# Kernel tuning notes

Hardware: AMD Instinct MI355X
Metric: run time of the kernel (lower is better)

## Reference

```python
import jax, jax.numpy as jnp
import numpy as np

N, E, F_IN, F_OUT, K, T = 100_000, 1_600_000, 64, 64, 2, 2


def setup_inputs() -> dict:
    key = jax.random.key(0)
    ks = jax.random.split(key, 7)
    s = 0.1
    return {
        "x": jax.random.normal(ks[0], (N, F_IN), jnp.float32),
        "edge_index": jax.random.randint(ks[1], (2, E), 0, N, dtype=jnp.int32),
        "edge_weight": jax.random.uniform(ks[2], (E,), jnp.float32),
        "init_weight": (jax.random.normal(ks[3], (K, F_IN, F_OUT), jnp.float32) * s),
        "weight": (jax.random.normal(ks[4], (T - 1, K, F_OUT, F_OUT), jnp.float32) * s),
        "root_weight": (jax.random.normal(ks[5], (T, K, F_IN, F_OUT), jnp.float32) * s),
        "bias": (jax.random.normal(ks[6], (T, K, F_OUT), jnp.float32) * s),
    }


def _gcn_norm(row, col, edge_weight, n):
    # PyG ARMAConv: gcn_norm with add_self_loops=False; degree on dst (col).
    deg = jax.ops.segment_sum(edge_weight, col, num_segments=n)
    dinv = jnp.where(deg > 0, jax.lax.rsqrt(jnp.maximum(deg, 1e-12)), 0.0)
    return dinv[row] * edge_weight * dinv[col]


def _propagate(out, row, col, norm, n):
    # out: [K, N, F] -> gather src rows, scale by norm, scatter-add at dst.
    msgs = out[:, row, :] * norm[None, :, None]  # [K, E, F]
    return jax.vmap(lambda m: jax.ops.segment_sum(m, col, num_segments=n))(msgs)


def reference(x, edge_index, edge_weight, init_weight, weight, root_weight, bias):
    n = x.shape[0]
    row, col = edge_index[0], edge_index[1]
    norm = _gcn_norm(row, col, edge_weight, n)
    out = x
    for t in range(T):
        if t == 0:
            out = jnp.einsum('nf,kfo->kno', x, init_weight)  # [K,N,F_out]
        else:
            out = jnp.einsum('kno,kop->knp', out, weight[t - 1])
        out = _propagate(out, row, col, norm, n)
        root = jnp.einsum('nf,kfo->kno', x, root_weight[t])  # dropout p=0 / eval
        out = jax.nn.relu(out + root + bias[t][:, None, :])
    return out.mean(axis=0)  # mean over stacks -> [N, F_out]
```

## Files before the change

### kernel.cpp

```cpp
#include <hip/hip_runtime.h>

#define NN 100000
#define EE 1600000
#define FF 64
#define KK 2

#define NBKT 391
#define BKW 256
#define CAP 8192
#define EPB 6250
#define P2CAP 6144

#define FIX 68719476736.0f
#define FIXINV (1.0/68719476736.0)

typedef unsigned long long ull;
typedef __attribute__((ext_vector_type(8))) short bf16x8;
typedef __attribute__((ext_vector_type(4))) float f32x4;
typedef __attribute__((ext_vector_type(2))) float f32x2;

__device__ inline unsigned pack_bf16x2(float a, float b) {
    unsigned ua = __float_as_uint(a), ub = __float_as_uint(b);
    ua = (ua + 0x7FFFu + ((ua >> 16) & 1u)) >> 16;
    ub = (ub + 0x7FFFu + ((ub >> 16) & 1u)) >> 16;
    return ua | (ub << 16);
}
__device__ inline float bf_lo(unsigned u) { return __uint_as_float(u << 16); }
__device__ inline float bf_hi(unsigned u) { return __uint_as_float(u & 0xFFFF0000u); }
__device__ inline short bf16_of(float f) {
    unsigned u = __float_as_uint(f);
    u = (u + 0x7FFFu + ((u >> 16) & 1u)) >> 16;
    return (short)u;
}
__device__ inline unsigned bf16_bits(float f) {
    unsigned u = __float_as_uint(f);
    return (u + 0x7FFFu + ((u >> 16) & 1u)) >> 16;
}
__device__ inline unsigned short fp8x2_of(float a, float b) {
    int p = __builtin_amdgcn_cvt_pk_fp8_f32(a, b, 0, false);
    return (unsigned short)(p & 0xFFFF);
}

__device__ inline bf16x8 load_bfrag(const float* __restrict__ W, int col, int kg, int c) {
    bf16x8 f;
    #pragma unroll
    for (int i = 0; i < 8; ++i)
        f[i] = bf16_of(W[(c*32 + kg*8 + i)*FF + col]);
    return f;
}

__global__ __launch_bounds__(512) void k_p1(const int* __restrict__ row,
                                            const int* __restrict__ col,
                                            const float* __restrict__ ew,
                                            int* __restrict__ gcnt,
                                            uint2* __restrict__ records) {
    __shared__ uint2 srt[EPB];
    __shared__ int colsS[EPB];
    __shared__ int histo[NBKT];
    __shared__ int lbase[NBKT];
    __shared__ int gbase[NBKT];
    __shared__ int cur[NBKT];
    __shared__ int tmp[512];
    int tid = threadIdx.x;
    for (int i = tid; i < NBKT; i += 512) histo[i] = 0;
    __syncthreads();
    int s0 = blockIdx.x * EPB;
    #pragma unroll 1
    for (int r = 0; r < 13; ++r) {
        int t = r*512 + tid;
        if (t < EPB) {
            int c = col[s0 + t];
            colsS[t] = c;
            atomicAdd(&histo[c >> 8], 1);
        }
    }
    __syncthreads();
    int v = (tid < NBKT) ? histo[tid] : 0;
    tmp[tid] = v;
    __syncthreads();
    #pragma unroll
    for (int s = 1; s < 512; s <<= 1) {
        int t = (tid >= s) ? tmp[tid - s] : 0;
        __syncthreads();
        tmp[tid] += t;
        __syncthreads();
    }
    if (tid < NBKT) {
        int ex = tmp[tid] - v;
        lbase[tid] = ex;
        cur[tid] = ex;
        gbase[tid] = atomicAdd(&gcnt[tid], v);
    }
    __syncthreads();
    #pragma unroll 1
    for (int r = 0; r < 13; ++r) {
        int t = r*512 + tid;
        if (t < EPB) {
            int i = s0 + t;
            int c = colsS[t];
            int b = c >> 8;
            int slot = atomicAdd(&cur[b], 1);
            srt[slot] = make_uint2(((unsigned)row[i] << 8) | (unsigned)(c & 255),
                                   __float_as_uint(ew[i]));
        }
    }
    __syncthreads();
    int wid = tid >> 6, lane = tid & 63;
    for (int b = wid; b < NBKT; b += 8) {
        int n = histo[b], lb = lbase[b];
        size_t gb = (size_t)b*CAP + gbase[b];
        for (int i = lane; i < n; i += 64) records[gb + i] = srt[lb + i];
    }
}

__global__ __launch_bounds__(512) void k_p2(const int* __restrict__ gcnt,
                                            const uint2* __restrict__ records,
                                            int* __restrict__ off,
                                            float* __restrict__ dinv,
                                            unsigned* __restrict__ edat) {
    __shared__ uint2 rstage[P2CAP];
    __shared__ ull hd[BKW];
    __shared__ int loff[BKW];
    __shared__ int cur[BKW];
    __shared__ int tmp[512];
    int tid = threadIdx.x;
    int b = blockIdx.x;
    int cnt = gcnt[b];
    int v = (tid < NBKT) ? gcnt[tid] : 0;
    tmp[tid] = v;
    __syncthreads();
    #pragma unroll
    for (int s = 1; s < 512; s <<= 1) {
        int t = (tid >= s) ? tmp[tid - s] : 0;
        __syncthreads();
        tmp[tid] += t;
        __syncthreads();
    }
    int obase = tmp[b] - cnt;
    if (b == 0 && tid == 0) off[NN] = EE;
    if (tid < BKW) hd[tid] = 0ull;
    __syncthreads();
    size_t rbase = (size_t)b * CAP;
    for (int j = tid; j < cnt; j += 512) {
        uint2 rec = records[rbase + j];
        if (j < P2CAP) rstage[j] = rec;
        int c8 = rec.x & 255;
        atomicAdd(&hd[c8], (1ull << 48) | (ull)(__uint_as_float(rec.y) * FIX));
    }
    __syncthreads();
    int hv = (tid < BKW) ? (int)(hd[tid] >> 48) : 0;
    tmp[tid] = hv;
    __syncthreads();
    #pragma unroll
    for (int s = 1; s < 512; s <<= 1) {
        int t = (tid >= s) ? tmp[tid - s] : 0;
        __syncthreads();
        tmp[tid] += t;
        __syncthreads();
    }
    if (tid < BKW) {
        int excl = tmp[tid] - hv;
        loff[tid] = excl;
        cur[tid] = excl;
        int node = b*BKW + tid;
        if (node < NN) {
            off[node] = obase + excl;
            float d = (float)((double)(hd[tid] & 0xFFFFFFFFFFFFull) * FIXINV);
            dinv[node] = d > 0.f ? rsqrtf(fmaxf(d, 1e-12f)) : 0.f;
        }
    }
    __syncthreads();
    for (int j = tid; j < cnt; j += 512) {
        uint2 rec = (j < P2CAP) ? rstage[j] : records[rbase + j];
        int c8 = rec.x & 255;
        int slot = atomicAdd(&cur[c8], 1);
        edat[obase + slot] = ((rec.x >> 8) << 15) |
                             (bf16_bits(__uint_as_float(rec.y)) & 0x7FFFu);
    }
}

__global__ __launch_bounds__(256) void k_proj3(const float* __restrict__ x,
                                               const float* __restrict__ iw,
                                               const float* __restrict__ rw,
                                               const float* __restrict__ bias,
                                               const float* __restrict__ dsc,
                                               unsigned short* __restrict__ hbf8,
                                               unsigned* __restrict__ rbf0,
                                               unsigned* __restrict__ rbf1) {
    int lane = threadIdx.x & 63, wid = threadIdx.x >> 6;
    int col16 = lane & 15, kg = lane >> 4;
    int col = wid*16 + col16;

    bf16x8 Bi[2][2], B0[2][2], B1[2][2];
    #pragma unroll
    for (int k = 0; k < 2; ++k)
        #pragma unroll
        for (int c = 0; c < 2; ++c) {
            Bi[k][c] = load_bfrag(iw + k*4096, col, kg, c);
            B0[k][c] = load_bfrag(rw + k*4096, col, kg, c);
            B1[k][c] = load_bfrag(rw + (2 + k)*4096, col, kg, c);
        }
    float b00 = bias[col],        b01 = bias[FF + col];
    float b10 = bias[2*FF + col], b11 = bias[3*FF + col];

    int base = blockIdx.x * 64;
    #pragma unroll
    for (int s = 0; s < 4; ++s) {
        int arow = base + s*16 + col16;
        if (arow >= NN) arow = NN - 1;
        const float* xp = x + arow*FF + kg*8;
        float4 v0 = *(const float4*)xp;
        float4 v1 = *(const float4*)(xp + 4);
        float4 v2 = *(const float4*)(xp + 32);
        float4 v3 = *(const float4*)(xp + 36);
        bf16x8 A0, A1;
        A0[0]=bf16_of(v0.x); A0[1]=bf16_of(v0.y); A0[2]=bf16_of(v0.z); A0[3]=bf16_of(v0.w);
        A0[4]=bf16_of(v1.x); A0[5]=bf16_of(v1.y); A0[6]=bf16_of(v1.z); A0[7]=bf16_of(v1.w);
        A1[0]=bf16_of(v2.x); A1[1]=bf16_of(v2.y); A1[2]=bf16_of(v2.z); A1[3]=bf16_of(v2.w);
        A1[4]=bf16_of(v3.x); A1[5]=bf16_of(v3.y); A1[6]=bf16_of(v3.z); A1[7]=bf16_of(v3.w);

        f32x4 hi0 = {0.f,0.f,0.f,0.f}, hi1 = {0.f,0.f,0.f,0.f};
        hi0 = __builtin_amdgcn_mfma_f32_16x16x32_bf16(A0, Bi[0][0], hi0, 0, 0, 0);
        hi0 = __builtin_amdgcn_mfma_f32_16x16x32_bf16(A1, Bi[0][1], hi0, 0, 0, 0);
        hi1 = __builtin_amdgcn_mfma_f32_16x16x32_bf16(A0, Bi[1][0], hi1, 0, 0, 0);
        hi1 = __builtin_amdgcn_mfma_f32_16x16x32_bf16(A1, Bi[1][1], hi1, 0, 0, 0);
        f32x4 r00 = {b00,b00,b00,b00}, r01 = {b01,b01,b01,b01};
        r00 = __builtin_amdgcn_mfma_f32_16x16x32_bf16(A0, B0[0][0], r00, 0, 0, 0);
        r00 = __builtin_amdgcn_mfma_f32_16x16x32_bf16(A1, B0[0][1], r00, 0, 0, 0);
        r01 = __builtin_amdgcn_mfma_f32_16x16x32_bf16(A0, B0[1][0], r01, 0, 0, 0);
        r01 = __builtin_amdgcn_mfma_f32_16x16x32_bf16(A1, B0[1][1], r01, 0, 0, 0);
        f32x4 r10 = {b10,b10,b10,b10}, r11 = {b11,b11,b11,b11};
        r10 = __builtin_amdgcn_mfma_f32_16x16x32_bf16(A0, B1[0][0], r10, 0, 0, 0);
        r10 = __builtin_amdgcn_mfma_f32_16x16x32_bf16(A1, B1[0][1], r10, 0, 0, 0);
        r11 = __builtin_amdgcn_mfma_f32_16x16x32_bf16(A0, B1[1][0], r11, 0, 0, 0);
        r11 = __builtin_amdgcn_mfma_f32_16x16x32_bf16(A1, B1[1][1], r11, 0, 0, 0);
        #pragma unroll
        for (int r = 0; r < 4; ++r) {
            int node = base + s*16 + kg*4 + r;
            if (node < NN) {
                float f = dsc[node];
                hbf8[(node<<6) + col]  = fp8x2_of(hi0[r]*f, hi1[r]*f);
                rbf0[(node<<6) + col] = pack_bf16x2(r00[r], r01[r]);
                rbf1[(node<<6) + col] = pack_bf16x2(r10[r], r11[r]);
            }
        }
    }
}

__global__ __launch_bounds__(256) void k_mml(const unsigned* __restrict__ in,
                                             const float* __restrict__ W,
                                             const float* __restrict__ dsc,
                                             unsigned short* __restrict__ outp8) {
    int lane = threadIdx.x & 63, wid = threadIdx.x >> 6;
    int col16 = lane & 15, kg = lane >> 4;
    int col = wid*16 + col16;

    bf16x8 B0[2], B1[2];
    #pragma unroll
    for (int c = 0; c < 2; ++c) {
        B0[c] = load_bfrag(W, col, kg, c);
        B1[c] = load_bfrag(W + 4096, col, kg, c);
    }
    int base = blockIdx.x * 64;
    #pragma unroll
    for (int s = 0; s < 4; ++s) {
        int arow = base + s*16 + col16;
        if (arow >= NN) arow = NN - 1;
        const unsigned* ip = in + arow*FF + kg*8;
        uint4 u0 = *(const uint4*)ip;
        uint4 u1 = *(const uint4*)(ip + 4);
        uint4 u2 = *(const uint4*)(ip + 32);
        uint4 u3 = *(const uint4*)(ip + 36);
        unsigned uu[16] = {u0.x,u0.y,u0.z,u0.w, u1.x,u1.y,u1.z,u1.w,
                           u2.x,u2.y,u2.z,u2.w, u3.x,u3.y,u3.z,u3.w};
        bf16x8 A00, A01, A10, A11;
        #pragma unroll
        for (int i = 0; i < 8; ++i) {
            A00[i] = (short)(uu[i] & 0xFFFFu);      A10[i] = (short)(uu[i] >> 16);
            A01[i] = (short)(uu[8+i] & 0xFFFFu);    A11[i] = (short)(uu[8+i] >> 16);
        }
        f32x4 a0 = {0.f, 0.f, 0.f, 0.f};
        f32x4 a1 = {0.f, 0.f, 0.f, 0.f};
        a0 = __builtin_amdgcn_mfma_f32_16x16x32_bf16(A00, B0[0], a0, 0, 0, 0);
        a0 = __builtin_amdgcn_mfma_f32_16x16x32_bf16(A01, B0[1], a0, 0, 0, 0);
        a1 = __builtin_amdgcn_mfma_f32_16x16x32_bf16(A10, B1[0], a1, 0, 0, 0);
        a1 = __builtin_amdgcn_mfma_f32_16x16x32_bf16(A11, B1[1], a1, 0, 0, 0);
        #pragma unroll
        for (int r = 0; r < 4; ++r) {
            int node = base + s*16 + kg*4 + r;
            if (node < NN) {
                float f = dsc[node];
                outp8[(node<<6) + col] = fp8x2_of(a0[r]*f, a1[r]*f);
            }
        }
    }
}

__global__ __launch_bounds__(512) void k_pull(const int* __restrict__ off,
                                              const unsigned* __restrict__ edat,
                                              const unsigned short* __restrict__ hbf,
                                              const unsigned* __restrict__ rbf,
                                              const float* __restrict__ dinv,
                                              unsigned* __restrict__ out_bf,
                                              float* __restrict__ out_f32,
                                              int final_mean) {
    __shared__ unsigned ech[8][64];
    int lane = threadIdx.x & 63;
    int sub = threadIdx.x >> 6;
    int n0 = (blockIdx.x * 8 + sub) * 2;
    if (n0 >= NN) return;
    int n1 = n0 + 1;

    int beg = off[n0], mid = off[n0+1], end = off[n0+2];
    float dc0 = dinv[n0], dc1 = dinv[n1];
    unsigned rv0 = rbf[(n0<<6) + lane];
    unsigned rv1 = rbf[(n1<<6) + lane];

    float pa0=0.f,pa1=0.f,pb0=0.f,pb1=0.f,pc0=0.f,pc1=0.f,pd0=0.f,pd1=0.f;
    float qa0=0.f,qa1=0.f,qb0=0.f,qb1=0.f,qc0=0.f,qc1=0.f,qd0=0.f,qd1=0.f;

    for (int base = beg; base < end; base += 64) {
        int rem = end - base;
        int cc = rem < 64 ? rem : 64;
        ech[sub][lane] = (lane < cc) ? edat[base + lane] : 0u;
        __builtin_amdgcn_wave_barrier();
        int midrel = mid - base;
        if (midrel < 0) midrel = 0;
        if (midrel > 64) midrel = 64;
        int padded = (cc + 7) & ~7;
        for (int q = 0; q < padded; q += 8) {
            unsigned e[8];
            #pragma unroll
            for (int i = 0; i < 8; ++i) e[i] = ech[sub][q + i];
            unsigned us[8];
            #pragma unroll
            for (int i = 0; i < 8; ++i)
                us[i] = hbf[((e[i] >> 15) << 6) + lane];
            if (q + 8 <= midrel) {
                #pragma unroll
                for (int i = 0; i < 8; ++i) {
                    float w = __uint_as_float((e[i] & 0x7FFFu) << 16);
                    f32x2 h = __builtin_amdgcn_cvt_pk_f32_fp8(us[i], false);
                    if      ((i & 3) == 0) { pa0 = fmaf(w, h.x, pa0); pa1 = fmaf(w, h.y, pa1); }
                    else if ((i & 3) == 1) { pb0 = fmaf(w, h.x, pb0); pb1 = fmaf(w, h.y, pb1); }
                    else if ((i & 3) == 2) { pc0 = fmaf(w, h.x, pc0); pc1 = fmaf(w, h.y, pc1); }
                    else                   { pd0 = fmaf(w, h.x, pd0); pd1 = fmaf(w, h.y, pd1); }
                }
            } else if (q >= midrel) {
                #pragma unroll
                for (int i = 0; i < 8; ++i) {
                    float w = __uint_as_float((e[i] & 0x7FFFu) << 16);
                    f32x2 h = __builtin_amdgcn_cvt_pk_f32_fp8(us[i], false);
                    if      ((i & 3) == 0) { qa0 = fmaf(w, h.x, qa0); qa1 = fmaf(w, h.y, qa1); }
                    else if ((i & 3) == 1) { qb0 = fmaf(w, h.x, qb0); qb1 = fmaf(w, h.y, qb1); }
                    else if ((i & 3) == 2) { qc0 = fmaf(w, h.x, qc0); qc1 = fmaf(w, h.y, qc1); }
                    else                   { qd0 = fmaf(w, h.x, qd0); qd1 = fmaf(w, h.y, qd1); }
                }
            } else {
                #pragma unroll
                for (int i = 0; i < 8; ++i) {
                    float w = __uint_as_float((e[i] & 0x7FFFu) << 16);
                    f32x2 h = __builtin_amdgcn_cvt_pk_f32_fp8(us[i], false);
                    if (q + i < midrel) {
                        if      ((i & 3) == 0) { pa0 = fmaf(w, h.x, pa0); pa1 = fmaf(w, h.y, pa1); }
                        else if ((i & 3) == 1) { pb0 = fmaf(w, h.x, pb0); pb1 = fmaf(w, h.y, pb1); }
                        else if ((i & 3) == 2) { pc0 = fmaf(w, h.x, pc0); pc1 = fmaf(w, h.y, pc1); }
                        else                   { pd0 = fmaf(w, h.x, pd0); pd1 = fmaf(w, h.y, pd1); }
                    } else {
                        if      ((i & 3) == 0) { qa0 = fmaf(w, h.x, qa0); qa1 = fmaf(w, h.y, qa1); }
                        else if ((i & 3) == 1) { qb0 = fmaf(w, h.x, qb0); qb1 = fmaf(w, h.y, qb1); }
                        else if ((i & 3) == 2) { qc0 = fmaf(w, h.x, qc0); qc1 = fmaf(w, h.y, qc1); }
                        else                   { qd0 = fmaf(w, h.x, qd0); qd1 = fmaf(w, h.y, qd1); }
                    }
                }
            }
        }
        __builtin_amdgcn_wave_barrier();
    }
    float s00 = fmaxf(fmaf(dc0, pa0 + pb0 + pc0 + pd0, bf_lo(rv0)), 0.f);
    float s01 = fmaxf(fmaf(dc0, pa1 + pb1 + pc1 + pd1, bf_hi(rv0)), 0.f);
    float s10 = fmaxf(fmaf(dc1, qa0 + qb0 + qc0 + qd0, bf_lo(rv1)), 0.f);
    float s11 = fmaxf(fmaf(dc1, qa1 + qb1 + qc1 + qd1, bf_hi(rv1)), 0.f);
    if (final_mean) {
        out_f32[n0*FF + lane] = 0.5f * (s00 + s01);
        out_f32[n1*FF + lane] = 0.5f * (s10 + s11);
    } else {
        out_bf[(n0<<6) + lane] = pack_bf16x2(s00, s01);
        out_bf[(n1<<6) + lane] = pack_bf16x2(s10, s11);
    }
}

extern "C" void kernel_launch(void* const* d_in, const int* in_sizes, int n_in,
                              void* d_out, int out_size, void* d_ws, size_t ws_size,
                              hipStream_t stream) {
    const float* x    = (const float*)d_in[0];
    const int*   ei   = (const int*)d_in[1];
    const float* ew   = (const float*)d_in[2];
    const float* iw   = (const float*)d_in[3];
    const float* w    = (const float*)d_in[4];
    const float* rw   = (const float*)d_in[5];
    const float* bias = (const float*)d_in[6];
    float* out = (float*)d_out;

    uint2* records = (uint2*)d_ws;
    unsigned* rbf1 = (unsigned*)records;
    unsigned short* hbf8 = (unsigned short*)(records + (size_t)NBKT*CAP);
    unsigned* gbf  = (unsigned*)(hbf8 + (NN<<6));
    unsigned* rbf0 = gbf + (NN<<6);
    unsigned* edat = rbf0 + (NN<<6);
    float* dinv    = (float*)(edat + EE);
    int*   off     = (int*)(dinv + NN);
    int*   gcnt    = off + NN + 1;

    const int* row = ei;
    const int* col = ei + EE;

    const int NB = (NN + 63) / 64;

    hipMemsetAsync(gcnt, 0, NBKT * sizeof(int), stream);
    k_p1<<<256, 512, 0, stream>>>(row, col, ew, gcnt, records);
    k_p2<<<NBKT, 512, 0, stream>>>(gcnt, records, off, dinv, edat);

    k_proj3<<<NB, 256, 0, stream>>>(x, iw, rw, bias, dinv, hbf8, rbf0, rbf1);

    k_pull<<<6250, 512, 0, stream>>>(off, edat, hbf8, rbf0, dinv, gbf, out, 0);

    k_mml<<<NB, 256, 0, stream>>>(gbf, w, dinv, hbf8);
    k_pull<<<6250, 512, 0, stream>>>(off, edat, hbf8, rbf1, dinv, gbf, out, 1);
}
```

Before: 184.8 us.

## Fuse root projection into pull kernel and widen edge records to uint2

Drops the precomputed bf16 root-term buffers. Each pull block now computes the root projection (x·root_weight + bias) for its 16 nodes with MFMA into shared memory before aggregating. Edge records grow from a packed 32-bit word to a uint2 holding a pre-shifted source offset and the full fp32 weight, which removes the unpacking work but doubles edge-stream traffic. This trades root-buffer writes and reads for recomputing from x in each pull, plus an extra block barrier.

```diff
diff --git a/kernel.cpp b/kernel.cpp
--- a/kernel.cpp
+++ b/kernel.cpp
@@ -3,7 +3,6 @@
 #define NN 100000
 #define EE 1600000
 #define FF 64
-#define KK 2
 
 #define NBKT 391
 #define BKW 256
@@ -32,10 +31,6 @@
     u = (u + 0x7FFFu + ((u >> 16) & 1u)) >> 16;
     return (short)u;
 }
-__device__ inline unsigned bf16_bits(float f) {
-    unsigned u = __float_as_uint(f);
-    return (u + 0x7FFFu + ((u >> 16) & 1u)) >> 16;
-}
 __device__ inline unsigned short fp8x2_of(float a, float b) {
     int p = __builtin_amdgcn_cvt_pk_fp8_f32(a, b, 0, false);
     return (unsigned short)(p & 0xFFFF);
@@ -47,6 +42,16 @@
     for (int i = 0; i < 8; ++i)
         f[i] = bf16_of(W[(c*32 + kg*8 + i)*FF + col]);
     return f;
+}
+__device__ inline void load_afrag(const float* __restrict__ xp, bf16x8& A0, bf16x8& A1) {
+    float4 v0 = *(const float4*)xp;
+    float4 v1 = *(const float4*)(xp + 4);
+    float4 v2 = *(const float4*)(xp + 32);
+    float4 v3 = *(const float4*)(xp + 36);
+    A0[0]=bf16_of(v0.x); A0[1]=bf16_of(v0.y); A0[2]=bf16_of(v0.z); A0[3]=bf16_of(v0.w);
+    A0[4]=bf16_of(v1.x); A0[5]=bf16_of(v1.y); A0[6]=bf16_of(v1.z); A0[7]=bf16_of(v1.w);
+    A1[0]=bf16_of(v2.x); A1[1]=bf16_of(v2.y); A1[2]=bf16_of(v2.z); A1[3]=bf16_of(v2.w);
+    A1[4]=bf16_of(v3.x); A1[5]=bf16_of(v3.y); A1[6]=bf16_of(v3.z); A1[7]=bf16_of(v3.w);
 }
 
 __global__ __launch_bounds__(512) void k_p1(const int* __restrict__ row,
@@ -117,10 +122,9 @@
                                             const uint2* __restrict__ records,
                                             int* __restrict__ off,
                                             float* __restrict__ dinv,
-                                            unsigned* __restrict__ edat) {
+                                            uint2* __restrict__ edat) {
     __shared__ uint2 rstage[P2CAP];
     __shared__ ull hd[BKW];
-    __shared__ int loff[BKW];
     __shared__ int cur[BKW];
     __shared__ int tmp[512];
     int tid = threadIdx.x;
@@ -160,7 +164,6 @@
     }
     if (tid < BKW) {
         int excl = tmp[tid] - hv;
-        loff[tid] = excl;
         cur[tid] = excl;
         int node = b*BKW + tid;
         if (node < NN) {
@@ -174,74 +177,44 @@
         uint2 rec = (j < P2CAP) ? rstage[j] : records[rbase + j];
         int c8 = rec.x & 255;
         int slot = atomicAdd(&cur[c8], 1);
-        edat[obase + slot] = ((rec.x >> 8) << 15) |
-                             (bf16_bits(__uint_as_float(rec.y)) & 0x7FFFu);
-    }
-}
-
-__global__ __launch_bounds__(256) void k_proj3(const float* __restrict__ x,
+        edat[obase + slot] = make_uint2((rec.x >> 8) << 6, rec.y);
+    }
+}
+
+__global__ __launch_bounds__(256) void k_projh(const float* __restrict__ x,
                                                const float* __restrict__ iw,
-                                               const float* __restrict__ rw,
-                                               const float* __restrict__ bias,
                                                const float* __restrict__ dsc,
-                                               unsigned short* __restrict__ hbf8,
-                                               unsigned* __restrict__ rbf0,
-                                               unsigned* __restrict__ rbf1) {
+                                               unsigned short* __restrict__ hbf8) {
     int lane = threadIdx.x & 63, wid = threadIdx.x >> 6;
     int col16 = lane & 15, kg = lane >> 4;
     int col = wid*16 + col16;
 
-    bf16x8 Bi[2][2], B0[2][2], B1[2][2];
+    bf16x8 Bi[2][2];
     #pragma unroll
     for (int k = 0; k < 2; ++k)
         #pragma unroll
-        for (int c = 0; c < 2; ++c) {
+        for (int c = 0; c < 2; ++c)
             Bi[k][c] = load_bfrag(iw + k*4096, col, kg, c);
-            B0[k][c] = load_bfrag(rw + k*4096, col, kg, c);
-            B1[k][c] = load_bfrag(rw + (2 + k)*4096, col, kg, c);
-        }
-    float b00 = bias[col],        b01 = bias[FF + col];
-    float b10 = bias[2*FF + col], b11 = bias[3*FF + col];
 
     int base = blockIdx.x * 64;
     #pragma unroll
     for (int s = 0; s < 4; ++s) {
         int arow = base + s*16 + col16;
         if (arow >= NN) arow = NN - 1;
-        const float* xp = x + arow*FF + kg*8;
-        float4 v0 = *(const float4*)xp;
-        float4 v1 = *(const float4*)(xp + 4);
-        float4 v2 = *(const float4*)(xp + 32);
-        float4 v3 = *(const float4*)(xp + 36);
         bf16x8 A0, A1;
-        A0[0]=bf16_of(v0.x); A0[1]=bf16_of(v0.y); A0[2]=bf16_of(v0.z); A0[3]=bf16_of(v0.w);
-        A0[4]=bf16_of(v1.x); A0[5]=bf16_of(v1.y); A0[6]=bf16_of(v1.z); A0[7]=bf16_of(v1.w);
-        A1[0]=bf16_of(v2.x); A1[1]=bf16_of(v2.y); A1[2]=bf16_of(v2.z); A1[3]=bf16_of(v2.w);
-        A1[4]=bf16_of(v3.x); A1[5]=bf16_of(v3.y); A1[6]=bf16_of(v3.z); A1[7]=bf16_of(v3.w);
-
-        f32x4 hi0 = {0.f,0.f,0.f,0.f}, hi1 = {0.f,0.f,0.f,0.f};
-        hi0 = __builtin_amdgcn_mfma_f32_16x16x32_bf16(A0, Bi[0][0], hi0, 0, 0, 0);
-        hi0 = __builtin_amdgcn_mfma_f32_16x16x32_bf16(A1, Bi[0][1], hi0, 0, 0, 0);
-        hi1 = __builtin_amdgcn_mfma_f32_16x16x32_bf16(A0, Bi[1][0], hi1, 0, 0, 0);
-        hi1 = __builtin_amdgcn_mfma_f32_16x16x32_bf16(A1, Bi[1][1], hi1, 0, 0, 0);
-        f32x4 r00 = {b00,b00,b00,b00}, r01 = {b01,b01,b01,b01};
-        r00 = __builtin_amdgcn_mfma_f32_16x16x32_bf16(A0, B0[0][0], r00, 0, 0, 0);
-        r00 = __builtin_amdgcn_mfma_f32_16x16x32_bf16(A1, B0[0][1], r00, 0, 0, 0);
-        r01 = __builtin_amdgcn_mfma_f32_16x16x32_bf16(A0, B0[1][0], r01, 0, 0, 0);
-        r01 = __builtin_amdgcn_mfma_f32_16x16x32_bf16(A1, B0[1][1], r01, 0, 0, 0);
-        f32x4 r10 = {b10,b10,b10,b10}, r11 = {b11,b11,b11,b11};
-        r10 = __builtin_amdgcn_mfma_f32_16x16x32_bf16(A0, B1[0][0], r10, 0, 0, 0);
-        r10 = __builtin_amdgcn_mfma_f32_16x16x32_bf16(A1, B1[0][1], r10, 0, 0, 0);
-        r11 = __builtin_amdgcn_mfma_f32_16x16x32_bf16(A0, B1[1][0], r11, 0, 0, 0);
-        r11 = __builtin_amdgcn_mfma_f32_16x16x32_bf16(A1, B1[1][1], r11, 0, 0, 0);
+        load_afrag(x + arow*FF + kg*8, A0, A1);
+
+        f32x4 h0 = {0.f,0.f,0.f,0.f}, h1 = {0.f,0.f,0.f,0.f};
+        h0 = __builtin_amdgcn_mfma_f32_16x16x32_bf16(A0, Bi[0][0], h0, 0, 0, 0);
+        h0 = __builtin_amdgcn_mfma_f32_16x16x32_bf16(A1, Bi[0][1], h0, 0, 0, 0);
+        h1 = __builtin_amdgcn_mfma_f32_16x16x32_bf16(A0, Bi[1][0], h1, 0, 0, 0);
+        h1 = __builtin_amdgcn_mfma_f32_16x16x32_bf16(A1, Bi[1][1], h1, 0, 0, 0);
         #pragma unroll
         for (int r = 0; r < 4; ++r) {
             int node = base + s*16 + kg*4 + r;
             if (node < NN) {
                 float f = dsc[node];
-                hbf8[(node<<6) + col]  = fp8x2_of(hi0[r]*f, hi1[r]*f);
-                rbf0[(node<<6) + col] = pack_bf16x2(r00[r], r01[r]);
-                rbf1[(node<<6) + col] = pack_bf16x2(r10[r], r11[r]);
+                hbf8[(node<<6) + col] = fp8x2_of(h0[r]*f, h1[r]*f);
             }
         }
     }
@@ -297,24 +270,45 @@
 }
 
 __global__ __launch_bounds__(512) void k_pull(const int* __restrict__ off,
-                                              const unsigned* __restrict__ edat,
+                                              const uint2* __restrict__ edat,
                                               const unsigned short* __restrict__ hbf,
-                                              const unsigned* __restrict__ rbf,
+                                              const float* __restrict__ x,
+                                              const float* __restrict__ rw,
+                                              const float* __restrict__ bias,
                                               const float* __restrict__ dinv,
                                               unsigned* __restrict__ out_bf,
                                               float* __restrict__ out_f32,
                                               int final_mean) {
-    __shared__ unsigned ech[8][64];
-    int lane = threadIdx.x & 63;
-    int sub = threadIdx.x >> 6;
-    int n0 = (blockIdx.x * 8 + sub) * 2;
-    if (n0 >= NN) return;
-    int n1 = n0 + 1;
-
+    __shared__ float rootf[2][16][FF];
+    __shared__ uint2 ech[8][64];
+    int tid = threadIdx.x;
+    int lane = tid & 63;
+    int sub = tid >> 6;
+    int nbase = blockIdx.x * 16;
+
+    {
+        int ct = sub & 3, kk = sub >> 2;
+        int col16 = lane & 15, kg = lane >> 4;
+        int c = ct*16 + col16;
+        bf16x8 Bc0 = load_bfrag(rw + kk*4096, c, kg, 0);
+        bf16x8 Bc1 = load_bfrag(rw + kk*4096, c, kg, 1);
+        bf16x8 A0, A1;
+        load_afrag(x + (nbase + col16)*FF + kg*8, A0, A1);
+        float bv = bias[kk*FF + c];
+        f32x4 acc = {bv, bv, bv, bv};
+        acc = __builtin_amdgcn_mfma_f32_16x16x32_bf16(A0, Bc0, acc, 0, 0, 0);
+        acc = __builtin_amdgcn_mfma_f32_16x16x32_bf16(A1, Bc1, acc, 0, 0, 0);
+        #pragma unroll
+        for (int r = 0; r < 4; ++r)
+            rootf[kk][kg*4 + r][c] = acc[r];
+    }
+    __syncthreads();
+
+    int n0 = nbase + sub*2, n1 = n0 + 1;
+    float r00 = rootf[0][sub*2][lane],     r01 = rootf[1][sub*2][lane];
+    float r10 = rootf[0][sub*2 + 1][lane], r11 = rootf[1][sub*2 + 1][lane];
+    float dc0 = dinv[n0], dc1 = dinv[n1];
     int beg = off[n0], mid = off[n0+1], end = off[n0+2];
-    float dc0 = dinv[n0], dc1 = dinv[n1];
-    unsigned rv0 = rbf[(n0<<6) + lane];
-    unsigned rv1 = rbf[(n1<<6) + lane];
 
     float pa0=0.f,pa1=0.f,pb0=0.f,pb1=0.f,pc0=0.f,pc1=0.f,pd0=0.f,pd1=0.f;
     float qa0=0.f,qa1=0.f,qb0=0.f,qb1=0.f,qc0=0.f,qc1=0.f,qd0=0.f,qd1=0.f;
@@ -322,24 +316,23 @@
     for (int base = beg; base < end; base += 64) {
         int rem = end - base;
         int cc = rem < 64 ? rem : 64;
-        ech[sub][lane] = (lane < cc) ? edat[base + lane] : 0u;
+        ech[sub][lane] = (lane < cc) ? edat[base + lane] : make_uint2(0u, 0u);
         __builtin_amdgcn_wave_barrier();
         int midrel = mid - base;
         if (midrel < 0) midrel = 0;
         if (midrel > 64) midrel = 64;
         int padded = (cc + 7) & ~7;
         for (int q = 0; q < padded; q += 8) {
-            unsigned e[8];
+            uint2 e[8];
             #pragma unroll
             for (int i = 0; i < 8; ++i) e[i] = ech[sub][q + i];
             unsigned us[8];
             #pragma unroll
-            for (int i = 0; i < 8; ++i)
-                us[i] = hbf[((e[i] >> 15) << 6) + lane];
+            for (int i = 0; i < 8; ++i) us[i] = hbf[e[i].x + lane];
             if (q + 8 <= midrel) {
                 #pragma unroll
                 for (int i = 0; i < 8; ++i) {
-                    float w = __uint_as_float((e[i] & 0x7FFFu) << 16);
+                    float w = __uint_as_float(e[i].y);
                     f32x2 h = __builtin_amdgcn_cvt_pk_f32_fp8(us[i], false);
                     if      ((i & 3) == 0) { pa0 = fmaf(w, h.x, pa0); pa1 = fmaf(w, h.y, pa1); }
                     else if ((i & 3) == 1) { pb0 = fmaf(w, h.x, pb0); pb1 = fmaf(w, h.y, pb1); }
@@ -349,7 +342,7 @@
             } else if (q >= midrel) {
                 #pragma unroll
                 for (int i = 0; i < 8; ++i) {
-                    float w = __uint_as_float((e[i] & 0x7FFFu) << 16);
+                    float w = __uint_as_float(e[i].y);
                     f32x2 h = __builtin_amdgcn_cvt_pk_f32_fp8(us[i], false);
                     if      ((i & 3) == 0) { qa0 = fmaf(w, h.x, qa0); qa1 = fmaf(w, h.y, qa1); }
                     else if ((i & 3) == 1) { qb0 = fmaf(w, h.x, qb0); qb1 = fmaf(w, h.y, qb1); }
@@ -359,7 +352,7 @@
             } else {
                 #pragma unroll
                 for (int i = 0; i < 8; ++i) {
-                    float w = __uint_as_float((e[i] & 0x7FFFu) << 16);
+                    float w = __uint_as_float(e[i].y);
                     f32x2 h = __builtin_amdgcn_cvt_pk_f32_fp8(us[i], false);
                     if (q + i < midrel) {
                         if      ((i & 3) == 0) { pa0 = fmaf(w, h.x, pa0); pa1 = fmaf(w, h.y, pa1); }
@@ -377,10 +370,10 @@
         }
         __builtin_amdgcn_wave_barrier();
     }
-    float s00 = fmaxf(fmaf(dc0, pa0 + pb0 + pc0 + pd0, bf_lo(rv0)), 0.f);
-    float s01 = fmaxf(fmaf(dc0, pa1 + pb1 + pc1 + pd1, bf_hi(rv0)), 0.f);
-    float s10 = fmaxf(fmaf(dc1, qa0 + qb0 + qc0 + qd0, bf_lo(rv1)), 0.f);
-    float s11 = fmaxf(fmaf(dc1, qa1 + qb1 + qc1 + qd1, bf_hi(rv1)), 0.f);
+    float s00 = fmaxf(fmaf(dc0, pa0 + pb0 + pc0 + pd0, r00), 0.f);
+    float s01 = fmaxf(fmaf(dc0, pa1 + pb1 + pc1 + pd1, r01), 0.f);
+    float s10 = fmaxf(fmaf(dc1, qa0 + qb0 + qc0 + qd0, r10), 0.f);
+    float s11 = fmaxf(fmaf(dc1, qa1 + qb1 + qc1 + qd1, r11), 0.f);
     if (final_mean) {
         out_f32[n0*FF + lane] = 0.5f * (s00 + s01);
         out_f32[n1*FF + lane] = 0.5f * (s10 + s11);
@@ -403,11 +396,9 @@
     float* out = (float*)d_out;
 
     uint2* records = (uint2*)d_ws;
-    unsigned* rbf1 = (unsigned*)records;
     unsigned short* hbf8 = (unsigned short*)(records + (size_t)NBKT*CAP);
     unsigned* gbf  = (unsigned*)(hbf8 + (NN<<6));
-    unsigned* rbf0 = gbf + (NN<<6);
-    unsigned* edat = rbf0 + (NN<<6);
+    uint2* edat    = (uint2*)(gbf + (NN<<6));
     float* dinv    = (float*)(edat + EE);
     int*   off     = (int*)(dinv + NN);
     int*   gcnt    = off + NN + 1;
@@ -421,10 +412,12 @@
     k_p1<<<256, 512, 0, stream>>>(row, col, ew, gcnt, records);
     k_p2<<<NBKT, 512, 0, stream>>>(gcnt, records, off, dinv, edat);
 
-    k_proj3<<<NB, 256, 0, stream>>>(x, iw, rw, bias, dinv, hbf8, rbf0, rbf1);
-
-    k_pull<<<6250, 512, 0, stream>>>(off, edat, hbf8, rbf0, dinv, gbf, out, 0);
+    k_projh<<<NB, 256, 0, stream>>>(x, iw, dinv, hbf8);
+
+    k_pull<<<6250, 512, 0, stream>>>(off, edat, hbf8, x, rw, bias,
+                                     dinv, gbf, out, 0);
 
     k_mml<<<NB, 256, 0, stream>>>(gbf, w, dinv, hbf8);
-    k_pull<<<6250, 512, 0, stream>>>(off, edat, hbf8, rbf1, dinv, gbf, out, 1);
-}
+    k_pull<<<6250, 512, 0, stream>>>(off, edat, hbf8, x, rw + 2*4096, bias + 2*FF,
+                                     dinv, gbf, out, 1);
+}
```

Result: slower. 223.9 us (+21.2%).
